# Kernel optimization log

Measured on AMD Instinct MI355X. Metric: run time of the kernel, lower is better.

## Reference

```python
import jax, jax.numpy as jnp
import numpy as np

D_MODEL = 1024
NUM_HEADS = 8
D_K = D_MODEL // NUM_HEADS


def setup_inputs() -> dict:
    key = jax.random.key(0)
    ks = jax.random.split(key, 11)
    B, S, D = 2, 2048, D_MODEL
    scale = 1.0 / np.sqrt(D)
    return {
        "Q": jax.random.normal(ks[0], (B, S, D), jnp.float32),
        "K": jax.random.normal(ks[1], (B, S, D), jnp.float32),
        "V": jax.random.normal(ks[2], (B, S, D), jnp.float32),
        # torch nn.Linear weights are stored (out_features, in_features)
        "Wq": jax.random.normal(ks[3], (D, D), jnp.float32) * scale,
        "bq": jnp.zeros((D,), jnp.float32),
        "Wk": jax.random.normal(ks[4], (D, D), jnp.float32) * scale,
        "bk": jnp.zeros((D,), jnp.float32),
        "Wv": jax.random.normal(ks[5], (D, D), jnp.float32) * scale,
        "bv": jnp.zeros((D,), jnp.float32),
        "Wo": jax.random.normal(ks[6], (D, D), jnp.float32) * scale,
        "bo": jnp.zeros((D,), jnp.float32),
    }


def reference(Q, K, V, Wq, bq, Wk, bk, Wv, bv, Wo, bo):
    B, S, D = Q.shape
    H, dk = NUM_HEADS, D_K
    # projections (torch Linear: x @ W.T + b), then split heads -> [B,H,S,dk]
    q = (Q @ Wq.T + bq).reshape(B, S, H, dk).transpose(0, 2, 1, 3)
    k = (K @ Wk.T + bk).reshape(B, S, H, dk).transpose(0, 2, 1, 3)
    v = (V @ Wv.T + bv).reshape(B, S, H, dk).transpose(0, 2, 1, 3)
    scores = jnp.einsum("bhqd,bhkd->bhqk", q, k) / jnp.sqrt(jnp.float32(dk))
    attn = jax.nn.softmax(scores, axis=-1)  # [B,H,S,S]
    ctx = jnp.einsum("bhqk,bhkd->bhqd", attn, v)
    concat = ctx.transpose(0, 2, 1, 3).reshape(B, S, D)
    out = concat @ Wo.T + bo
    return out, attn
```

## Files before the change

### kernel.cpp

```cpp
#include <hip/hip_runtime.h>

#define S_LEN 2048
#define DMODEL 1024
#define NHEADS 8
#define DK 128
#define BATCH 2

typedef _Float16 h16;
typedef __attribute__((ext_vector_type(8))) _Float16 half8v;
typedef __attribute__((ext_vector_type(4))) float float4v;

#define GLD16(gp, lp)                                                  \
  __builtin_amdgcn_global_load_lds(                                    \
      (const __attribute__((address_space(1))) void*)(gp),             \
      (__attribute__((address_space(3))) void*)(lp), 16, 0, 0)

#define BAR_VM0()                                                       \
  do {                                                                  \
    asm volatile("s_waitcnt vmcnt(0) lgkmcnt(0)\ns_barrier" ::: "memory"); \
    __builtin_amdgcn_sched_barrier(0);                                  \
  } while (0)
#define BAR_VM16()                                                      \
  do {                                                                  \
    asm volatile("s_waitcnt vmcnt(16) lgkmcnt(0)\ns_barrier" ::: "memory"); \
    __builtin_amdgcn_sched_barrier(0);                                  \
  } while (0)
#define BAR_LGKM()                                                      \
  do {                                                                  \
    asm volatile("s_waitcnt lgkmcnt(0)\ns_barrier" ::: "memory");       \
    __builtin_amdgcn_sched_barrier(0);                                  \
  } while (0)

__global__ __launch_bounds__(256) void cvt_all(
    const float* __restrict__ q, const float* __restrict__ k, const float* __restrict__ v,
    const float* __restrict__ wq, const float* __restrict__ wk, const float* __restrict__ wv,
    const float* __restrict__ wo,
    h16* __restrict__ dq, h16* __restrict__ dk, h16* __restrict__ dv,
    h16* __restrict__ dwq, h16* __restrict__ dwk, h16* __restrict__ dwv,
    h16* __restrict__ dwo) {
  int i = blockIdx.x * 256 + threadIdx.x;
  const float* src;
  h16* dst;
  int off;
  if (i < 1572864) {
    int seg = i >> 19;
    off = i & 524287;
    src = seg == 0 ? q : (seg == 1 ? k : v);
    dst = seg == 0 ? dq : (seg == 1 ? dk : dv);
  } else {
    int j = i - 1572864;
    int seg = j >> 17;
    off = j & 131071;
    src = seg == 0 ? wq : (seg == 1 ? wk : (seg == 2 ? wv : wo));
    dst = seg == 0 ? dwq : (seg == 1 ? dwk : (seg == 2 ? dwv : dwo));
  }
  const float4* s = (const float4*)src + (size_t)off * 2;
  float4 a = s[0], b = s[1];
  half8v h = {(h16)a.x, (h16)a.y, (h16)a.z, (h16)a.w,
              (h16)b.x, (h16)b.y, (h16)b.z, (h16)b.w};
  *((half8v*)dst + off) = h;
}

__global__ __launch_bounds__(256) void qkv_gemm(
    const h16* __restrict__ qf, const h16* __restrict__ kf, const h16* __restrict__ vf,
    const h16* __restrict__ wq, const h16* __restrict__ wk, const h16* __restrict__ wv,
    const float* __restrict__ bq, const float* __restrict__ bk, const float* __restrict__ bv,
    h16* __restrict__ qh, h16* __restrict__ kh, h16* __restrict__ vt) {
  __shared__ h16 As[2][128 * 32];
  __shared__ h16 Bs[2][128 * 32];

  const int z = blockIdx.z;
  const h16* A = z == 0 ? qf : (z == 1 ? kf : vf);
  const h16* Bw = z == 0 ? wq : (z == 1 ? wk : wv);
  const float* bias = z == 0 ? bq : (z == 1 ? bk : bv);
  h16* outp = z == 0 ? qh : (z == 1 ? kh : vt);

  const int t = threadIdx.x, lane = t & 63, w = t >> 6;
  const int m0 = blockIdx.y * 128, n0 = blockIdx.x * 128;
  const int wm = (w >> 1) * 64, wn = (w & 1) * 64;
  const int lcol = lane & 15, lquad = lane >> 4;

  float4v acc[4][4];
  for (int i = 0; i < 4; ++i)
    for (int j = 0; j < 4; ++j) acc[i][j] = {0.f, 0.f, 0.f, 0.f};

#define QKV_STAGE(S, P)                                                    \
  for (int j = 0; j < 2; ++j) {                                            \
    int i = w * 2 + j;                                                     \
    int row = i * 16 + (lane >> 2);                                        \
    int c4 = (lane & 3) ^ ((row >> 1) & 3);                                \
    GLD16(A + (size_t)(m0 + row) * 1024 + (S) * 32 + c4 * 8, As[P] + i * 512); \
    GLD16(Bw + (size_t)(n0 + row) * 1024 + (S) * 32 + c4 * 8, Bs[P] + i * 512); \
  }

  QKV_STAGE(0, 0);
  BAR_VM0();

  for (int s = 0; s < 32; ++s) {
    int sn = s + 1 < 32 ? s + 1 : s;
    QKV_STAGE(sn, (s + 1) & 1);

    const h16* Ar = As[s & 1];
    const h16* Br = Bs[s & 1];
    half8v af[4], bf[4];
    for (int mi = 0; mi < 4; ++mi) {
      int r = wm + mi * 16 + lcol;
      af[mi] = *(const half8v*)(Ar + r * 32 + ((lquad ^ ((r >> 1) & 3)) << 3));
    }
    for (int ni = 0; ni < 4; ++ni) {
      int r = wn + ni * 16 + lcol;
      bf[ni] = *(const half8v*)(Br + r * 32 + ((lquad ^ ((r >> 1) & 3)) << 3));
    }
    for (int mi = 0; mi < 4; ++mi)
      for (int ni = 0; ni < 4; ++ni)
        acc[mi][ni] = __builtin_amdgcn_mfma_f32_16x16x32_f16(af[mi], bf[ni],
                                                             acc[mi][ni], 0, 0, 0);
    BAR_VM0();
  }

  for (int ni = 0; ni < 4; ++ni) {
    int gn = n0 + wn + ni * 16 + lcol;
    float bvv = bias[gn];
    int hh = gn >> 7, dv = gn & 127;
    for (int mi = 0; mi < 4; ++mi) {
      int gmb = m0 + wm + mi * 16 + lquad * 4;
      for (int r = 0; r < 4; ++r) {
        int gm = gmb + r;
        float v = acc[mi][ni][r] + bvv;
        int b = gm >> 11, sdx = gm & 2047;
        if (z < 2)
          outp[((size_t)(b * NHEADS + hh) * S_LEN + sdx) * DK + dv] = (h16)v;
        else
          outp[((size_t)(b * NHEADS + hh) * DK + dv) * S_LEN + sdx] = (h16)v;
      }
    }
  }
}

__global__ __launch_bounds__(256) void out_gemm(const h16* __restrict__ A,
                                                const h16* __restrict__ Bw,
                                                const float* __restrict__ bias,
                                                float* __restrict__ C) {
  __shared__ h16 As[2][64 * 32];
  __shared__ h16 Bs[2][128 * 32];

  const int t = threadIdx.x, lane = t & 63, w = t >> 6;
  const int m0 = blockIdx.y * 64, n0 = blockIdx.x * 128;
  const int wm = (w >> 1) * 32, wn = (w & 1) * 64;
  const int lcol = lane & 15, lquad = lane >> 4;

  float4v acc[2][4];
  for (int i = 0; i < 2; ++i)
    for (int j = 0; j < 4; ++j) acc[i][j] = {0.f, 0.f, 0.f, 0.f};

#define OUT_STAGE(S, P)                                                    \
  {                                                                        \
    int row = w * 16 + (lane >> 2);                                        \
    int c4 = (lane & 3) ^ ((row >> 1) & 3);                                \
    GLD16(A + (size_t)(m0 + row) * 1024 + (S) * 32 + c4 * 8, As[P] + w * 512); \
    for (int j = 0; j < 2; ++j) {                                          \
      int i = w * 2 + j;                                                   \
      int row2 = i * 16 + (lane >> 2);                                     \
      int c42 = (lane & 3) ^ ((row2 >> 1) & 3);                            \
      GLD16(Bw + (size_t)(n0 + row2) * 1024 + (S) * 32 + c42 * 8, Bs[P] + i * 512); \
    }                                                                      \
  }

  OUT_STAGE(0, 0);
  BAR_VM0();

  for (int s = 0; s < 32; ++s) {
    int sn = s + 1 < 32 ? s + 1 : s;
    OUT_STAGE(sn, (s + 1) & 1);

    const h16* Ar = As[s & 1];
    const h16* Br = Bs[s & 1];
    half8v af[2], bf[4];
    for (int mi = 0; mi < 2; ++mi) {
      int r = wm + mi * 16 + lcol;
      af[mi] = *(const half8v*)(Ar + r * 32 + ((lquad ^ ((r >> 1) & 3)) << 3));
    }
    for (int ni = 0; ni < 4; ++ni) {
      int r = wn + ni * 16 + lcol;
      bf[ni] = *(const half8v*)(Br + r * 32 + ((lquad ^ ((r >> 1) & 3)) << 3));
    }
    for (int mi = 0; mi < 2; ++mi)
      for (int ni = 0; ni < 4; ++ni)
        acc[mi][ni] = __builtin_amdgcn_mfma_f32_16x16x32_f16(af[mi], bf[ni],
                                                             acc[mi][ni], 0, 0, 0);
    BAR_VM0();
  }

  for (int ni = 0; ni < 4; ++ni) {
    int gn = n0 + wn + ni * 16 + lcol;
    float bvv = bias[gn];
    for (int mi = 0; mi < 2; ++mi) {
      int gmb = m0 + wm + mi * 16 + lquad * 4;
      for (int r = 0; r < 4; ++r)
        C[(size_t)(gmb + r) * 1024 + gn] = acc[mi][ni][r] + bvv;
    }
  }
}

__device__ inline void attn_bid(int& bh, int& q0) {
  int id = blockIdx.y * 32 + blockIdx.x;
  int xcd = id & 7, rank = id >> 3;
  bh = xcd + 8 * (rank >> 5);
  q0 = (rank & 31) * 64;
}

__global__ __launch_bounds__(256, 2) void attn_fused(
    const h16* __restrict__ qh, const h16* __restrict__ kh,
    const h16* __restrict__ vt, float* __restrict__ attn,
    h16* __restrict__ ctxb) {
  __shared__ h16 Ks[2][64 * 128];
  __shared__ h16 Vts[2][128 * 64];
  __shared__ h16 Ps[64 * 72];

  const int t = threadIdx.x, lane = t & 63, w = t >> 6;
  const int lcol = lane & 15, lquad = lane >> 4;
  int bh, q0;
  attn_bid(bh, q0);
  const int b = bh >> 3, h = bh & 7;
  const float scale = 0.08838834764831845f;

#define STAGE_K(KT, BUF)                                                     \
  for (int j = 0; j < 4; ++j) {                                              \
    int i = w * 4 + j;                                                       \
    int row = i * 4 + (lane >> 4);                                           \
    int c4 = (lane & 15) ^ (row & 7);                                        \
    GLD16(kh + ((size_t)bh * S_LEN + (KT) * 64 + row) * DK + c4 * 8,         \
          (BUF) + i * 512);                                                  \
  }
#define STAGE_V(KT, BUF)                                                     \
  for (int j = 0; j < 4; ++j) {                                              \
    int i = w * 4 + j;                                                       \
    int row = i * 8 + (lane >> 3);                                           \
    int c4 = (lane & 7) ^ (row & 7);                                         \
    GLD16(vt + ((size_t)bh * DK + row) * S_LEN + (KT) * 64 + c4 * 8,         \
          (BUF) + i * 512);                                                  \
  }

  for (int j = 0; j < 4; ++j) {
    int i = w * 4 + j;
    int row = i * 4 + (lane >> 4);
    int c4 = (lane & 15) ^ (row & 7);
    GLD16(qh + ((size_t)bh * S_LEN + q0 + row) * DK + c4 * 8, Ks[0] + i * 512);
  }
  BAR_VM0();
  STAGE_K(0, Ks[1]);
  half8v aq[4][4];
  for (int mi = 0; mi < 4; ++mi) {
    int r = mi * 16 + lcol;
    for (int ks = 0; ks < 4; ++ks)
      aq[mi][ks] = *(const half8v*)(Ks[0] + r * 128 + (((ks * 4 + lquad) ^ (r & 7)) << 3));
  }
  BAR_VM0();

  float ls[4][4];
  for (int mi = 0; mi < 4; ++mi)
    for (int rr = 0; rr < 4; ++rr) ls[mi][rr] = 0.f;

  for (int s = 0; s < 32; ++s) {
    int sn = s + 1 < 32 ? s + 1 : s;
    STAGE_K(sn, Ks[s & 1]);

    const h16* Kr = Ks[(s + 1) & 1];
    float4v sacc[4];
    for (int mi = 0; mi < 4; ++mi) sacc[mi] = {0.f, 0.f, 0.f, 0.f};
    int r = w * 16 + lcol;
    for (int ks = 0; ks < 4; ++ks) {
      half8v bk = *(const half8v*)(Kr + r * 128 + (((ks * 4 + lquad) ^ (r & 7)) << 3));
      for (int mi = 0; mi < 4; ++mi)
        sacc[mi] = __builtin_amdgcn_mfma_f32_16x16x32_f16(aq[mi][ks], bk, sacc[mi], 0, 0, 0);
    }
    for (int mi = 0; mi < 4; ++mi)
      for (int rr = 0; rr < 4; ++rr) ls[mi][rr] += __expf(sacc[mi][rr] * scale);
    BAR_VM0();
  }

  float* red = (float*)Ps;
  for (int mi = 0; mi < 4; ++mi)
    for (int rr = 0; rr < 4; ++rr) {
      float vsum = ls[mi][rr];
      for (int off = 1; off < 16; off <<= 1) vsum += __shfl_xor(vsum, off);
      if (lcol == 0) red[w * 64 + mi * 16 + lquad * 4 + rr] = vsum;
    }
  __syncthreads();
  float il[4][4];
  for (int mi = 0; mi < 4; ++mi)
    for (int rr = 0; rr < 4; ++rr) {
      int row = mi * 16 + lquad * 4 + rr;
      il[mi][rr] = 1.f / (red[row] + red[64 + row] + red[128 + row] + red[192 + row]);
    }

  float4v cacc[4][2];
  for (int mi = 0; mi < 4; ++mi)
    for (int nd = 0; nd < 2; ++nd) cacc[mi][nd] = {0.f, 0.f, 0.f, 0.f};

  float* abase = attn + ((size_t)bh * S_LEN + q0 + lquad * 4) * S_LEN + w * 16 + lcol;

  STAGE_K(0, Ks[0]);
  STAGE_V(0, Vts[0]);
  BAR_VM0();

  for (int s = 0; s < 32; ++s) {
    int p = s & 1;
    int sn = s + 1 < 32 ? s + 1 : s;
    STAGE_K(sn, Ks[p ^ 1]);
    STAGE_V(sn, Vts[p ^ 1]);

    const h16* Kr = Ks[p];
    float4v sacc[4];
    for (int mi = 0; mi < 4; ++mi) sacc[mi] = {0.f, 0.f, 0.f, 0.f};
    {
      int r = w * 16 + lcol;
      for (int ks = 0; ks < 4; ++ks) {
        half8v bk = *(const half8v*)(Kr + r * 128 + (((ks * 4 + lquad) ^ (r & 7)) << 3));
        for (int mi = 0; mi < 4; ++mi)
          sacc[mi] = __builtin_amdgcn_mfma_f32_16x16x32_f16(aq[mi][ks], bk, sacc[mi], 0, 0, 0);
      }
    }

    h16* Psw = Ps + lquad * 4 * 72 + w * 16 + lcol;
    float* ab = abase + (size_t)s * 64;
    for (int mi = 0; mi < 4; ++mi)
      for (int rr = 0; rr < 4; ++rr) {
        float pv = __expf(sacc[mi][rr] * scale) * il[mi][rr];
        ab[(size_t)(mi * 16 + rr) * S_LEN] = pv;
        Psw[(mi * 16 + rr) * 72] = (h16)pv;
      }

    BAR_LGKM();

    {
      const h16* Vr = Vts[p];
      half8v ap[4][2];
      for (int mi = 0; mi < 4; ++mi)
        for (int k2 = 0; k2 < 2; ++k2)
          ap[mi][k2] = *(const half8v*)(Ps + (mi * 16 + lcol) * 72 + k2 * 32 + lquad * 8);
      for (int nd = 0; nd < 2; ++nd) {
        int r = w * 32 + nd * 16 + lcol;
        for (int k2 = 0; k2 < 2; ++k2) {
          half8v bv = *(const half8v*)(Vr + r * 64 + (((k2 * 4 + lquad) ^ (r & 7)) << 3));
          for (int mi = 0; mi < 4; ++mi)
            cacc[mi][nd] = __builtin_amdgcn_mfma_f32_16x16x32_f16(ap[mi][k2], bv,
                                                                  cacc[mi][nd], 0, 0, 0);
        }
      }
    }

    BAR_VM16();
  }

  h16* cb = ctxb + ((size_t)b * S_LEN + q0 + lquad * 4) * DMODEL + h * DK + w * 32;
  for (int mi = 0; mi < 4; ++mi)
    for (int nd = 0; nd < 2; ++nd)
      for (int rr = 0; rr < 4; ++rr)
        cb[(size_t)(mi * 16 + rr) * DMODEL + nd * 16 + lcol] = (h16)cacc[mi][nd][rr];
}

extern "C" void kernel_launch(void* const* d_in, const int* in_sizes, int n_in,
                              void* d_out, int out_size, void* d_ws, size_t ws_size,
                              hipStream_t stream) {
  const float* Q  = (const float*)d_in[0];
  const float* K  = (const float*)d_in[1];
  const float* V  = (const float*)d_in[2];
  const float* Wq = (const float*)d_in[3];
  const float* bq = (const float*)d_in[4];
  const float* Wk = (const float*)d_in[5];
  const float* bk = (const float*)d_in[6];
  const float* Wv = (const float*)d_in[7];
  const float* bv = (const float*)d_in[8];
  const float* Wo = (const float*)d_in[9];
  const float* bo = (const float*)d_in[10];

  float* out  = (float*)d_out;
  float* attn = out + (size_t)BATCH * S_LEN * DMODEL;

  const size_t NTOK = (size_t)BATCH * S_LEN * DMODEL;
  const size_t NW = (size_t)DMODEL * DMODEL;
  h16* qf  = (h16*)d_ws;
  h16* kf  = qf + NTOK;
  h16* vf  = kf + NTOK;
  h16* wqh = vf + NTOK;
  h16* wkh = wqh + NW;
  h16* wvh = wkh + NW;
  h16* woh = wvh + NW;
  h16* qh  = woh + NW;
  h16* kh  = qh + NTOK;
  h16* vt  = kh + NTOK;
  h16* ctxb = qf;

  dim3 gb(256);
  cvt_all<<<dim3(8192), gb, 0, stream>>>(Q, K, V, Wq, Wk, Wv, Wo,
                                         qf, kf, vf, wqh, wkh, wvh, woh);
  qkv_gemm<<<dim3(8, 32, 3), gb, 0, stream>>>(qf, kf, vf, wqh, wkh, wvh,
                                              bq, bk, bv, qh, kh, vt);
  attn_fused<<<dim3(32, 16), gb, 0, stream>>>(qh, kh, vt, attn, ctxb);
  out_gemm<<<dim3(8, 64), gb, 0, stream>>>(ctxb, woh, bo, out);
}
```

Baseline: 478.8 us.

## Fuse fp32-to-fp16 activation conversion into QKV GEMM and remap block order

Drops the separate conversion pass over the Q/K/V activations. The QKV GEMM now loads fp32 tiles straight into LDS with an XOR swizzle and converts them to fp16 when building the MFMA fragments. The weight conversion kernel shrinks to weights only. Both GEMMs also remap block indices so consecutive blocks cover different N tiles, which should improve L2 reuse of the A rows. The cost is twice the LDS traffic and capacity for the A tiles, plus conversion instructions in the inner loop; the context buffer gets its own workspace region.

Result: slower. 499.4 us (+4.3%).

```diff
diff --git a/kernel.cpp b/kernel.cpp
--- a/kernel.cpp
+++ b/kernel.cpp
@@ -31,29 +31,15 @@
     __builtin_amdgcn_sched_barrier(0);                                  \
   } while (0)
 
-__global__ __launch_bounds__(256) void cvt_all(
-    const float* __restrict__ q, const float* __restrict__ k, const float* __restrict__ v,
-    const float* __restrict__ wq, const float* __restrict__ wk, const float* __restrict__ wv,
-    const float* __restrict__ wo,
-    h16* __restrict__ dq, h16* __restrict__ dk, h16* __restrict__ dv,
+__global__ __launch_bounds__(256) void cvt_w(
+    const float* __restrict__ wq, const float* __restrict__ wk,
+    const float* __restrict__ wv, const float* __restrict__ wo,
     h16* __restrict__ dwq, h16* __restrict__ dwk, h16* __restrict__ dwv,
     h16* __restrict__ dwo) {
   int i = blockIdx.x * 256 + threadIdx.x;
-  const float* src;
-  h16* dst;
-  int off;
-  if (i < 1572864) {
-    int seg = i >> 19;
-    off = i & 524287;
-    src = seg == 0 ? q : (seg == 1 ? k : v);
-    dst = seg == 0 ? dq : (seg == 1 ? dk : dv);
-  } else {
-    int j = i - 1572864;
-    int seg = j >> 17;
-    off = j & 131071;
-    src = seg == 0 ? wq : (seg == 1 ? wk : (seg == 2 ? wv : wo));
-    dst = seg == 0 ? dwq : (seg == 1 ? dwk : (seg == 2 ? dwv : dwo));
-  }
+  int seg = i >> 17, off = i & 131071;
+  const float* src = seg == 0 ? wq : (seg == 1 ? wk : (seg == 2 ? wv : wo));
+  h16* dst = seg == 0 ? dwq : (seg == 1 ? dwk : (seg == 2 ? dwv : dwo));
   const float4* s = (const float4*)src + (size_t)off * 2;
   float4 a = s[0], b = s[1];
   half8v h = {(h16)a.x, (h16)a.y, (h16)a.z, (h16)a.w,
@@ -62,21 +48,25 @@
 }
 
 __global__ __launch_bounds__(256) void qkv_gemm(
-    const h16* __restrict__ qf, const h16* __restrict__ kf, const h16* __restrict__ vf,
+    const float* __restrict__ qf, const float* __restrict__ kf, const float* __restrict__ vf,
     const h16* __restrict__ wq, const h16* __restrict__ wk, const h16* __restrict__ wv,
     const float* __restrict__ bq, const float* __restrict__ bk, const float* __restrict__ bv,
     h16* __restrict__ qh, h16* __restrict__ kh, h16* __restrict__ vt) {
-  __shared__ h16 As[2][128 * 32];
+  __shared__ float Asf[2][128 * 32];
   __shared__ h16 Bs[2][128 * 32];
 
-  const int z = blockIdx.z;
-  const h16* A = z == 0 ? qf : (z == 1 ? kf : vf);
+  int lin = blockIdx.x + blockIdx.y * 8 + blockIdx.z * 256;
+  int virt = (lin & 7) * 96 + (lin >> 3);
+  const int n0 = (virt & 7) * 128;
+  const int m0 = ((virt >> 3) & 31) * 128;
+  const int z = virt >> 8;
+
+  const float* A32 = z == 0 ? qf : (z == 1 ? kf : vf);
   const h16* Bw = z == 0 ? wq : (z == 1 ? wk : wv);
   const float* bias = z == 0 ? bq : (z == 1 ? bk : bv);
   h16* outp = z == 0 ? qh : (z == 1 ? kh : vt);
 
   const int t = threadIdx.x, lane = t & 63, w = t >> 6;
-  const int m0 = blockIdx.y * 128, n0 = blockIdx.x * 128;
   const int wm = (w >> 1) * 64, wn = (w & 1) * 64;
   const int lcol = lane & 15, lquad = lane >> 4;
 
@@ -84,12 +74,17 @@
   for (int i = 0; i < 4; ++i)
     for (int j = 0; j < 4; ++j) acc[i][j] = {0.f, 0.f, 0.f, 0.f};
 
-#define QKV_STAGE(S, P)                                                    \
-  for (int j = 0; j < 2; ++j) {                                            \
-    int i = w * 2 + j;                                                     \
-    int row = i * 16 + (lane >> 2);                                        \
-    int c4 = (lane & 3) ^ ((row >> 1) & 3);                                \
-    GLD16(A + (size_t)(m0 + row) * 1024 + (S) * 32 + c4 * 8, As[P] + i * 512); \
+#define QKV_STAGE(S, P)                                                       \
+  for (int j = 0; j < 4; ++j) {                                               \
+    int i = w * 4 + j;                                                        \
+    int row = i * 8 + (lane >> 3);                                            \
+    int cs = (lane & 7) ^ (row & 7);                                          \
+    GLD16(A32 + (size_t)(m0 + row) * 1024 + (S) * 32 + cs * 4, Asf[P] + i * 256); \
+  }                                                                           \
+  for (int j = 0; j < 2; ++j) {                                               \
+    int i = w * 2 + j;                                                        \
+    int row = i * 16 + (lane >> 2);                                           \
+    int c4 = (lane & 3) ^ ((row >> 1) & 3);                                   \
     GLD16(Bw + (size_t)(n0 + row) * 1024 + (S) * 32 + c4 * 8, Bs[P] + i * 512); \
   }
 
@@ -100,12 +95,17 @@
     int sn = s + 1 < 32 ? s + 1 : s;
     QKV_STAGE(sn, (s + 1) & 1);
 
-    const h16* Ar = As[s & 1];
+    const float* Ar = Asf[s & 1];
     const h16* Br = Bs[s & 1];
     half8v af[4], bf[4];
     for (int mi = 0; mi < 4; ++mi) {
       int r = wm + mi * 16 + lcol;
-      af[mi] = *(const half8v*)(Ar + r * 32 + ((lquad ^ ((r >> 1) & 3)) << 3));
+      int s0 = (2 * lquad) ^ (r & 7);
+      int s1 = (2 * lquad + 1) ^ (r & 7);
+      float4v x = *(const float4v*)(Ar + r * 32 + s0 * 4);
+      float4v y = *(const float4v*)(Ar + r * 32 + s1 * 4);
+      af[mi] = {(h16)x[0], (h16)x[1], (h16)x[2], (h16)x[3],
+                (h16)y[0], (h16)y[1], (h16)y[2], (h16)y[3]};
     }
     for (int ni = 0; ni < 4; ++ni) {
       int r = wn + ni * 16 + lcol;
@@ -144,8 +144,12 @@
   __shared__ h16 As[2][64 * 32];
   __shared__ h16 Bs[2][128 * 32];
 
+  int lin = blockIdx.x + blockIdx.y * 8;
+  int virt = (lin & 7) * 64 + (lin >> 3);
+  const int n0 = (virt & 7) * 128;
+  const int m0 = (virt >> 3) * 64;
+
   const int t = threadIdx.x, lane = t & 63, w = t >> 6;
-  const int m0 = blockIdx.y * 64, n0 = blockIdx.x * 128;
   const int wm = (w >> 1) * 32, wn = (w & 1) * 64;
   const int lcol = lane & 15, lquad = lane >> 4;
 
@@ -380,22 +384,18 @@
 
   const size_t NTOK = (size_t)BATCH * S_LEN * DMODEL;
   const size_t NW = (size_t)DMODEL * DMODEL;
-  h16* qf  = (h16*)d_ws;
-  h16* kf  = qf + NTOK;
-  h16* vf  = kf + NTOK;
-  h16* wqh = vf + NTOK;
+  h16* wqh = (h16*)d_ws;
   h16* wkh = wqh + NW;
   h16* wvh = wkh + NW;
   h16* woh = wvh + NW;
   h16* qh  = woh + NW;
   h16* kh  = qh + NTOK;
   h16* vt  = kh + NTOK;
-  h16* ctxb = qf;
+  h16* ctxb = vt + NTOK;
 
   dim3 gb(256);
-  cvt_all<<<dim3(8192), gb, 0, stream>>>(Q, K, V, Wq, Wk, Wv, Wo,
-                                         qf, kf, vf, wqh, wkh, wvh, woh);
-  qkv_gemm<<<dim3(8, 32, 3), gb, 0, stream>>>(qf, kf, vf, wqh, wkh, wvh,
+  cvt_w<<<dim3(2048), gb, 0, stream>>>(Wq, Wk, Wv, Wo, wqh, wkh, wvh, woh);
+  qkv_gemm<<<dim3(8, 32, 3), gb, 0, stream>>>(Q, K, V, wqh, wkh, wvh,
                                               bq, bk, bv, qh, kh, vt);
   attn_fused<<<dim3(32, 16), gb, 0, stream>>>(qh, kh, vt, attn, ctxb);
   out_gemm<<<dim3(8, 64), gb, 0, stream>>>(ctxb, woh, bo, out);
```
